# Performance work log

Measured on AMD Instinct MI355X. Metric: run time of the kernel, lower is better.

Reference implementation:

```python
import jax, jax.numpy as jnp
import numpy as np
import math

N_TERMS = 10
TWO_PI = 2.0 * math.pi


def _zernike_tables(n_terms):
    # Terms in the exact order of the torch loops: n in [0,n_terms), m in range(-n, n+1, 2).
    terms = []
    for n in range(n_terms):
        for m in range(-n, n + 1, 2):
            terms.append((n, m))
    T = len(terms)  # n_terms*(n_terms+1)/2 = 55 for n_terms=10
    C = np.zeros((T, n_terms), dtype=np.float32)  # C[t, p] = coeff of rho**p for term t
    ms = np.zeros(T, dtype=np.float32)
    for t, (n, m) in enumerate(terms):
        am = abs(m)
        for k in range((n - am) // 2 + 1):
            c = ((-1) ** k) * math.factorial(n - k) / (
                math.factorial(k)
                * math.factorial((n + am) // 2 - k)
                * math.factorial((n - am) // 2 - k)
            )
            C[t, n - 2 * k] += c
        ms[t] = m
    return C, ms


_C_NP, _MS_NP = _zernike_tables(N_TERMS)


def setup_inputs() -> dict:
    key = jax.random.key(0)
    x = jax.random.normal(key, (32, 1, 1024, 1024), dtype=jnp.float32)
    return {"x": x}


def reference(x) -> jnp.ndarray:
    # FFT features
    fft_image = jnp.fft.rfft2(x)                    # [B,1,H,Wr], Wr = W//2+1
    magnitude = jnp.abs(fft_image)
    phase = jnp.angle(fft_image)
    pu = jnp.where(phase < 0, phase + TWO_PI, phase)  # "unwrapped" phase

    # Phase gradients (torch.gradient semantics == jnp.gradient: central diff, one-sided edges)
    grad_y, grad_x = jnp.gradient(pu, axis=(2, 3))

    # Zernike coefficients over the phase map grid
    B, _, H, Wr = pu.shape
    yv = jnp.linspace(-1.0, 1.0, H)
    xv = jnp.linspace(-1.0, 1.0, Wr)
    gy, gx = jnp.meshgrid(yv, xv, indexing="ij")   # [H,Wr]
    rho = jnp.sqrt(gx ** 2 + gy ** 2)
    theta = jnp.arctan2(gy, gx)
    mask = (rho <= 1.0).astype(pu.dtype)

    C = jnp.asarray(_C_NP)                          # [T,P]
    ms = jnp.asarray(_MS_NP)                        # [T]
    powers = jnp.arange(N_TERMS, dtype=pu.dtype)    # rho**0 .. rho**(n_terms-1)
    rho_pows = rho[None] ** powers[:, None, None]   # [P,H,Wr]
    R = jnp.einsum("tp,phw->thw", C, rho_pows)     # radial polynomials, [T,H,Wr]
    mt = ms[:, None, None] * theta[None]
    ang = jnp.where(ms[:, None, None] >= 0, jnp.cos(mt), jnp.sin(-mt))
    Z = R * ang                                     # [T,H,Wr]

    pm = pu[:, 0] * mask                            # [B,H,Wr]
    coeffs = jnp.einsum("bhw,thw->bt", pm, Z) / jnp.sum(mask)  # [B,T]

    # Slope stats (torch .std is unbiased -> ddof=1)
    slope_stats = jnp.concatenate(
        [
            grad_x.mean(axis=(2, 3)),
            grad_y.mean(axis=(2, 3)),
            grad_x.std(axis=(2, 3), ddof=1),
            grad_y.std(axis=(2, 3), ddof=1),
        ],
        axis=1,
    )                                               # [B,4]

    freq_features = jnp.max(magnitude, axis=(2, 3))  # [B,1]

    return jnp.concatenate([coeffs, slope_stats, freq_features], axis=1)  # [B,60]
```

## Files before the change

kernel.cpp:

```cpp
#include <hip/hip_runtime.h>
#include <math.h>

#define BATCH 32
#define HH 1024
#define WW 1024
#define WR 513
#define NPIX (HH * WR)
#define TWO_PI_F 6.28318530717958647692f

#define LGKM_SYNC() __asm__ __volatile__("s_waitcnt lgkmcnt(0)" ::: "memory")

__device__ __forceinline__ float2 cadd(float2 a, float2 b) { return make_float2(a.x + b.x, a.y + b.y); }
__device__ __forceinline__ float2 csub(float2 a, float2 b) { return make_float2(a.x - b.x, a.y - b.y); }
__device__ __forceinline__ float2 cmul(float2 a, float2 b) {
    return make_float2(a.x * b.x - a.y * b.y, a.x * b.y + a.y * b.x);
}

__device__ __forceinline__ float fast_atan2f(float y, float x) {
    float ax = __builtin_fabsf(x), ay = __builtin_fabsf(y);
    float mx = fmaxf(ax, ay), mn = fminf(ax, ay);
    float a = mn * __builtin_amdgcn_rcpf(mx);
    float s = a * a;
    float r = fmaf(fmaf(fmaf(fmaf(0.0208351f, s, -0.085133f), s, 0.180141f),
                        s, -0.3302995f), s, 0.999866f) * a;
    if (ay > ax) r = 1.5707963268f - r;
    if (x < 0.0f) r = 3.1415926536f - r;
    return (y < 0.0f) ? -r : r;
}

__device__ __forceinline__ constexpr int ridx(int k) { return ((k & 3) << 2) | (k >> 2); }

__device__ __forceinline__ void fft16_ip(float2* d) {
    const float2 Wt1[4] = {{1.f, 0.f},
                           {0.92387953f, -0.38268343f},
                           {0.70710678f, -0.70710678f},
                           {0.38268343f, -0.92387953f}};
    const float2 Wt2[4] = {{1.f, 0.f},
                           {0.70710678f, -0.70710678f},
                           {0.f, -1.f},
                           {-0.70710678f, -0.70710678f}};
    const float2 Wt3[4] = {{1.f, 0.f},
                           {0.38268343f, -0.92387953f},
                           {-0.70710678f, -0.70710678f},
                           {-0.92387953f, 0.38268343f}};
#pragma unroll
    for (int t = 0; t < 4; ++t) {
        float2 x0 = d[t], x1 = d[t + 4], x2 = d[t + 8], x3 = d[t + 12];
        float2 a0 = cadd(x0, x2), a1 = csub(x0, x2), a2 = cadd(x1, x3), a3 = csub(x1, x3);
        d[t]      = cadd(a0, a2);
        d[t + 4]  = cmul(make_float2(a1.x + a3.y, a1.y - a3.x), Wt1[t]);
        d[t + 8]  = cmul(csub(a0, a2), Wt2[t]);
        d[t + 12] = cmul(make_float2(a1.x - a3.y, a1.y + a3.x), Wt3[t]);
    }
#pragma unroll
    for (int r = 0; r < 4; ++r) {
        float2 x0 = d[4 * r], x1 = d[4 * r + 1], x2 = d[4 * r + 2], x3 = d[4 * r + 3];
        float2 e0 = cadd(x0, x2), e1 = csub(x0, x2), e2 = cadd(x1, x3), e3 = csub(x1, x3);
        d[4 * r]     = cadd(e0, e2);
        d[4 * r + 1] = make_float2(e1.x + e3.y, e1.y - e3.x);
        d[4 * r + 2] = csub(e0, e2);
        d[4 * r + 3] = make_float2(e1.x - e3.y, e1.y + e3.x);
    }
}

__device__ __forceinline__ void twiddle_tree(float2 T, float2* Wt) {
    Wt[1] = T;
    Wt[2] = cmul(T, T);
    Wt[3] = cmul(Wt[2], T);
    Wt[4] = cmul(Wt[2], Wt[2]);
    Wt[5] = cmul(Wt[4], Wt[1]);
    Wt[6] = cmul(Wt[4], Wt[2]);
    Wt[7] = cmul(Wt[4], Wt[3]);
    Wt[8] = cmul(Wt[4], Wt[4]);
    Wt[9]  = cmul(Wt[8], Wt[1]);
    Wt[10] = cmul(Wt[8], Wt[2]);
    Wt[11] = cmul(Wt[8], Wt[3]);
    Wt[12] = cmul(Wt[8], Wt[4]);
    Wt[13] = cmul(Wt[8], Wt[5]);
    Wt[14] = cmul(Wt[8], Wt[6]);
    Wt[15] = cmul(Wt[8], Wt[7]);
}

__device__ __forceinline__ void wave_fft1024(float2* v, float2* sb, int lane) {
    fft16_ip(v);
    float s, c;
    __sincosf(-TWO_PI_F * (float)lane * (1.0f / 1024.0f), &s, &c);
    float2 Wt[16];
    twiddle_tree(make_float2(c, s), Wt);
#pragma unroll
    for (int k2 = 1; k2 < 16; ++k2) v[ridx(k2)] = cmul(v[ridx(k2)], Wt[k2]);
    const int k2p = lane & 15, qp = lane >> 4;
#pragma unroll
    for (int k2 = 0; k2 < 16; ++k2) sb[(k2 << 6) | (lane ^ k2)] = v[ridx(k2)];
    LGKM_SYNC();
#pragma unroll
    for (int m = 0; m < 16; ++m) v[m] = sb[(k2p << 6) | ((4 * m + qp) ^ k2p)];
    LGKM_SYNC();
    fft16_ip(v);
    __sincosf(-TWO_PI_F * (float)qp * (1.0f / 64.0f), &s, &c);
    twiddle_tree(make_float2(c, s), Wt);
#pragma unroll
    for (int km = 1; km < 16; ++km) v[ridx(km)] = cmul(v[ridx(km)], Wt[km]);
    const bool hi2 = (lane & 32) != 0, hi1 = (lane & 16) != 0;
#pragma unroll
    for (int m = 0; m < 16; ++m) {
        float2 a = v[m];
        float2 o = make_float2(__shfl_xor(a.x, 32, 64), __shfl_xor(a.y, 32, 64));
        float2 s1 = hi2 ? csub(o, a) : cadd(a, o);
        if (hi2 && hi1) s1 = make_float2(s1.y, -s1.x);
        float2 o2 = make_float2(__shfl_xor(s1.x, 16, 64), __shfl_xor(s1.y, 16, 64));
        v[m] = hi1 ? csub(o2, s1) : cadd(s1, o2);
    }
}

__global__ __launch_bounds__(256, 4) void row_fft_kernel(const float* __restrict__ x,
                                                         float2* __restrict__ rf2) {
    __shared__ float2 buf[4][1024];
    const int t = threadIdx.x, w = t >> 6, lane = t & 63;
    const int b = blockIdx.x >> 7;
    const int h0 = (blockIdx.x & 127) * 8;
    const float* r0 = x + ((long long)b * HH + h0 + 2 * w) * (long long)WW;
    const float* r1 = r0 + WW;
    float2 v[16];
#pragma unroll
    for (int j = 0; j < 16; ++j) v[j] = make_float2(r0[lane + 64 * j], r1[lane + 64 * j]);
    float2* mybuf = &buf[w][0];
    wave_fft1024(v, mybuf, lane);
    const int kq = 2 * ((lane >> 4) & 1) + ((lane >> 5) & 1);
    const int kbase = (lane & 15) + 256 * kq;
#pragma unroll
    for (int m = 0; m < 16; ++m) mybuf[kbase + 16 * m] = v[ridx(m)];
    __syncthreads();
    for (int idx = t; idx < 513 * 8; idx += 256) {
        int k = idx >> 3, j = idx & 7, p = j >> 1, which = j & 1;
        float2 zk = buf[p][k];
        float2 zn = buf[p][(1024 - k) & 1023];
        float2 val = which ? make_float2(0.5f * (zk.y + zn.y), 0.5f * (zn.x - zk.x))
                           : make_float2(0.5f * (zk.x + zn.x), 0.5f * (zk.y - zn.y));
        rf2[((long long)b * WR + k) * 1024 + h0 + j] = val;
    }
}

__device__ __forceinline__ constexpr int brev5(int k) {
    return ((k & 1) << 4) | ((k & 2) << 2) | (k & 4) | ((k & 8) >> 2) | ((k & 16) >> 4);
}

__device__ __forceinline__ void fft32_dif(float2* d) {
    const float2 TW[16] = {
        {1.f, 0.f},
        {0.98078528f, -0.19509032f},
        {0.92387953f, -0.38268343f},
        {0.83146961f, -0.55557023f},
        {0.70710678f, -0.70710678f},
        {0.55557023f, -0.83146961f},
        {0.38268343f, -0.92387953f},
        {0.19509032f, -0.98078528f},
        {0.f, -1.f},
        {-0.19509032f, -0.98078528f},
        {-0.38268343f, -0.92387953f},
        {-0.55557023f, -0.83146961f},
        {-0.70710678f, -0.70710678f},
        {-0.83146961f, -0.55557023f},
        {-0.92387953f, -0.38268343f},
        {-0.98078528f, -0.19509032f}};
#pragma unroll
    for (int s = 0; s < 5; ++s) {
        const int h = 16 >> s;
#pragma unroll
        for (int b = 0; b < 32; b += 2 * h) {
#pragma unroll
            for (int j = 0; j < h; ++j) {
                float2 a = d[b + j], c = d[b + j + h];
                d[b + j]     = cadd(a, c);
                d[b + j + h] = cmul(csub(a, c), TW[j << s]);
            }
        }
    }
}

__global__ __launch_bounds__(64, 4) void col_fft_kernel(float2* __restrict__ rf2,
                                                        float* __restrict__ magmax) {
    __shared__ float2 sb[2 * 1056];
    const int lane = threadIdx.x;
    const int n1 = lane & 31, row = lane >> 5;
    const long long fbase = (long long)blockIdx.x * 2;
    const long long fid = fbase + row;
    const float2* src = rf2 + fbase * 1024;

    float2 d[32];
#pragma unroll
    for (int j = 0; j < 32; ++j) d[j] = src[row * 1024 + n1 + 32 * j];

    fft32_dif(d);

    float s0, c0;
    __sincosf(-TWO_PI_F * (float)n1 * (1.0f / 1024.0f), &s0, &c0);
    const float2 Tn = make_float2(c0, s0);
    float2 ww = Tn;
#pragma unroll
    for (int k1 = 1; k1 < 32; ++k1) {
        d[brev5(k1)] = cmul(d[brev5(k1)], ww);
        if (k1 < 31) ww = cmul(ww, Tn);
    }

    float2* myLDS = sb + row * 1056;
#pragma unroll
    for (int k1 = 0; k1 < 32; ++k1) myLDS[33 * k1 + n1] = d[brev5(k1)];
    LGKM_SYNC();
#pragma unroll
    for (int j = 0; j < 32; ++j) d[j] = myLDS[33 * n1 + j];

    fft32_dif(d);

    float* pu = (float*)(rf2 + fid * 1024);
    float mmax = 0.0f;
#pragma unroll
    for (int k2 = 0; k2 < 32; ++k2) {
        float2 z = d[brev5(k2)];
        mmax = fmaxf(mmax, __builtin_amdgcn_sqrtf(z.x * z.x + z.y * z.y));
        float ph = fast_atan2f(z.y, z.x);
        pu[32 * k2 + n1] = (ph < 0.0f) ? ph + TWO_PI_F : ph;
    }
#pragma unroll
    for (int off = 16; off; off >>= 1) mmax = fmaxf(mmax, __shfl_xor(mmax, off, 64));
    if (n1 == 0) atomicMax((int*)(magmax + (int)(fid / WR)), __float_as_int(mmax));
}

#define WRED(var, idx)                                                     \
    {                                                                      \
        float r_ = var;                                                    \
        _Pragma("unroll")                                                  \
        for (int off_ = 32; off_; off_ >>= 1) r_ += __shfl_down(r_, off_); \
        if (lane == 0) red[wv * 64 + (idx)] = r_;                          \
    }

#define ZPIX(VV, YVV)                                                          \
    {                                                                          \
        const float yv_ = (YVV);                                               \
        const float r2_ = xv2 + yv_ * yv_;                                     \
        if (r2_ <= 1.0f) {                                                     \
            cnt += 1.0f;                                                       \
            const float rho = sqrtf(r2_);                                      \
            const float inv = rsqrtf(r2_);                                     \
            const float c1 = xv * inv;                                         \
            const float s1 = yv_ * inv;                                        \
            const float c2 = 2.f * c1 * c1 - 1.f;                              \
            const float c3 = 2.f * c1 * c2 - c1;                               \
            const float c4 = 2.f * c1 * c3 - c2;                               \
            const float c5 = 2.f * c1 * c4 - c3;                               \
            const float c6 = 2.f * c1 * c5 - c4;                               \
            const float c7 = 2.f * c1 * c6 - c5;                               \
            const float c8 = 2.f * c1 * c7 - c6;                               \
            const float c9 = 2.f * c1 * c8 - c7;                               \
            const float s2 = 2.f * c1 * s1;                                    \
            const float s3 = 2.f * c1 * s2 - s1;                               \
            const float s4 = 2.f * c1 * s3 - s2;                               \
            const float s5 = 2.f * c1 * s4 - s3;                               \
            const float s6 = 2.f * c1 * s5 - s4;                               \
            const float s7 = 2.f * c1 * s6 - s5;                               \
            const float s8 = 2.f * c1 * s7 - s6;                               \
            const float s9 = 2.f * c1 * s8 - s7;                               \
            const float w0 = (VV), w1 = w0 * rho, w2 = w1 * rho, w3 = w2 * rho,\
                        w4 = w3 * rho, w5 = w4 * rho, w6 = w5 * rho,           \
                        w7 = w6 * rho, w8 = w7 * rho, w9 = w8 * rho;           \
            a00 += w0;                                                         \
            a11 += w1 * c1;                                                    \
            a20 += w2;      a22 += w2 * c2;                                    \
            a31 += w3 * c1; a33 += w3 * c3;                                    \
            a40 += w4;      a42 += w4 * c2; a44 += w4 * c4;                    \
            a51 += w5 * c1; a53 += w5 * c3; a55 += w5 * c5;                    \
            a60 += w6;      a62 += w6 * c2; a64 += w6 * c4; a66 += w6 * c6;    \
            a71 += w7 * c1; a73 += w7 * c3; a75 += w7 * c5; a77 += w7 * c7;    \
            a80 += w8;      a82 += w8 * c2; a84 += w8 * c4; a86 += w8 * c6;    \
            a88 += w8 * c8;                                                    \
            a91 += w9 * c1; a93 += w9 * c3; a95 += w9 * c5; a97 += w9 * c7;    \
            a99 += w9 * c9;                                                    \
            b11 += w1 * s1;                                                    \
            b22 += w2 * s2;                                                    \
            b31 += w3 * s1; b33 += w3 * s3;                                    \
            b42 += w4 * s2; b44 += w4 * s4;                                    \
            b51 += w5 * s1; b53 += w5 * s3; b55 += w5 * s5;                    \
            b62 += w6 * s2; b64 += w6 * s4; b66 += w6 * s6;                    \
            b71 += w7 * s1; b73 += w7 * s3; b75 += w7 * s5; b77 += w7 * s7;    \
            b82 += w8 * s2; b84 += w8 * s4; b86 += w8 * s6; b88 += w8 * s8;    \
            b91 += w9 * s1; b93 += w9 * s3; b95 += w9 * s5; b97 += w9 * s7;    \
            b99 += w9 * s9;                                                    \
        }                                                                      \
    }

__global__ __launch_bounds__(256, 2) void stats_kernel(float* __restrict__ pu) {
    __shared__ float red[4 * 64];
    const int b = blockIdx.y;
    const int k0 = blockIdx.x * 9;
    const float* base = pu + (long long)b * WR * 2048;
    float a00 = 0.f, a11 = 0.f, a20 = 0.f, a22 = 0.f, a31 = 0.f, a33 = 0.f,
          a40 = 0.f, a42 = 0.f, a44 = 0.f, a51 = 0.f, a53 = 0.f, a55 = 0.f,
          a60 = 0.f, a62 = 0.f, a64 = 0.f, a66 = 0.f, a71 = 0.f, a73 = 0.f,
          a75 = 0.f, a77 = 0.f, a80 = 0.f, a82 = 0.f, a84 = 0.f, a86 = 0.f,
          a88 = 0.f, a91 = 0.f, a93 = 0.f, a95 = 0.f, a97 = 0.f, a99 = 0.f;
    float b11 = 0.f, b22 = 0.f, b31 = 0.f, b33 = 0.f, b42 = 0.f, b44 = 0.f,
          b51 = 0.f, b53 = 0.f, b55 = 0.f, b62 = 0.f, b64 = 0.f, b66 = 0.f,
          b71 = 0.f, b73 = 0.f, b75 = 0.f, b77 = 0.f, b82 = 0.f, b84 = 0.f,
          b86 = 0.f, b88 = 0.f, b91 = 0.f, b93 = 0.f, b95 = 0.f, b97 = 0.f,
          b99 = 0.f;
    float sgx = 0.f, sgx2 = 0.f, sgy = 0.f, sgy2 = 0.f, cnt = 0.f;

    const int h4 = threadIdx.x * 4;
    const float yv0 = -1.0f + (2.0f / 1023.0f) * (float)h4;
    const float ystep = 2.0f / 1023.0f;

    for (int kk = 0; kk < 9; ++kk) {
        const int k = k0 + kk;
        const float* rowc = base + (long long)k * 2048;
        const float xv = -1.0f + (1.0f / 256.0f) * (float)k;
        const float xv2 = xv * xv;

        const float4 vc = *reinterpret_cast<const float4*>(rowc + h4);
        float4 gx4;
        if (k == 0) {
            const float4 vp = *reinterpret_cast<const float4*>(rowc + 2048 + h4);
            gx4 = make_float4(vp.x - vc.x, vp.y - vc.y, vp.z - vc.z, vp.w - vc.w);
        } else if (k == WR - 1) {
            const float4 vm = *reinterpret_cast<const float4*>(rowc - 2048 + h4);
            gx4 = make_float4(vc.x - vm.x, vc.y - vm.y, vc.z - vm.z, vc.w - vm.w);
        } else {
            const float4 vm = *reinterpret_cast<const float4*>(rowc - 2048 + h4);
            const float4 vp = *reinterpret_cast<const float4*>(rowc + 2048 + h4);
            gx4 = make_float4(0.5f * (vp.x - vm.x), 0.5f * (vp.y - vm.y),
                              0.5f * (vp.z - vm.z), 0.5f * (vp.w - vm.w));
        }
        const float left  = rowc[(h4 > 0) ? h4 - 1 : 0];
        const float right = rowc[(h4 < 1020) ? h4 + 4 : 1023];
        const float gy0 = (h4 == 0)    ? vc.y - vc.x : 0.5f * (vc.y - left);
        const float gy1 = 0.5f * (vc.z - vc.x);
        const float gy2 = 0.5f * (vc.w - vc.y);
        const float gy3 = (h4 == 1020) ? vc.w - vc.z : 0.5f * (right - vc.z);

        sgx  += gx4.x + gx4.y + gx4.z + gx4.w;
        sgx2 += gx4.x * gx4.x + gx4.y * gx4.y + gx4.z * gx4.z + gx4.w * gx4.w;
        sgy  += gy0 + gy1 + gy2 + gy3;
        sgy2 += gy0 * gy0 + gy1 * gy1 + gy2 * gy2 + gy3 * gy3;

        ZPIX(vc.x, yv0);
        ZPIX(vc.y, yv0 + ystep);
        ZPIX(vc.z, yv0 + 2.0f * ystep);
        ZPIX(vc.w, yv0 + 3.0f * ystep);
    }

    const int wv = threadIdx.x >> 6, lane = threadIdx.x & 63;
    WRED(a00, 0);  WRED(a11, 1);  WRED(a20, 2);  WRED(a22, 3);  WRED(a31, 4);
    WRED(a33, 5);  WRED(a40, 6);  WRED(a42, 7);  WRED(a44, 8);  WRED(a51, 9);
    WRED(a53, 10); WRED(a55, 11); WRED(a60, 12); WRED(a62, 13); WRED(a64, 14);
    WRED(a66, 15); WRED(a71, 16); WRED(a73, 17); WRED(a75, 18); WRED(a77, 19);
    WRED(a80, 20); WRED(a82, 21); WRED(a84, 22); WRED(a86, 23); WRED(a88, 24);
    WRED(a91, 25); WRED(a93, 26); WRED(a95, 27); WRED(a97, 28); WRED(a99, 29);
    WRED(b11, 30); WRED(b22, 31); WRED(b31, 32); WRED(b33, 33); WRED(b42, 34);
    WRED(b44, 35); WRED(b51, 36); WRED(b53, 37); WRED(b55, 38); WRED(b62, 39);
    WRED(b64, 40); WRED(b66, 41); WRED(b71, 42); WRED(b73, 43); WRED(b75, 44);
    WRED(b77, 45); WRED(b82, 46); WRED(b84, 47); WRED(b86, 48); WRED(b88, 49);
    WRED(b91, 50); WRED(b93, 51); WRED(b95, 52); WRED(b97, 53); WRED(b99, 54);
    WRED(sgx, 55); WRED(sgx2, 56); WRED(sgy, 57); WRED(sgy2, 58); WRED(cnt, 59);
    __syncthreads();
    const int t = threadIdx.x;
    if (t < 60) {
        float s = red[t] + red[64 + t] + red[128 + t] + red[192 + t];
        pu[((long long)(b * 57 + blockIdx.x)) * 2048 + 1024 + t] = s;
    }
}

__device__ int moment_index(int p, int a, int is_cos) {
    int ai = 0;
    for (int pp = 0; pp < 10; ++pp)
        for (int aa = (pp & 1); aa <= pp; aa += 2) {
            if (is_cos && pp == p && aa == a) return ai;
            ++ai;
        }
    for (int pp = 1; pp < 10; ++pp)
        for (int aa = ((pp & 1) ? 1 : 2); aa <= pp; aa += 2) {
            if (!is_cos && pp == p && aa == a) return ai;
            ++ai;
        }
    return 0;
}

__device__ float factf(int n) {
    float f = 1.0f;
    for (int i = 2; i <= n; ++i) f *= (float)i;
    return f;
}

__global__ void finalize_kernel(const float* __restrict__ pu,
                                const float* __restrict__ magmax,
                                float* __restrict__ out) {
    __shared__ float abf[64];
    const int b = blockIdx.x;
    const int j = threadIdx.x;
    if (j < 60) {
        float s = 0.0f;
        for (int i = 0; i < 57; ++i)
            s += pu[((long long)(b * 57 + i)) * 2048 + 1024 + j];
        abf[j] = s;
    }
    __syncthreads();
    if (j >= 60) return;
    const float NF = (float)NPIX;
    float val;
    if (j < 55) {
        int tt = j, n = 0;
        while (tt >= n + 1) { tt -= (n + 1); ++n; }
        int m = -n + 2 * tt;
        int am = m < 0 ? -m : m;
        float s = 0.0f;
        for (int k = 0; k <= (n - am) / 2; ++k) {
            float c = factf(n - k) /
                      (factf(k) * factf((n + am) / 2 - k) * factf((n - am) / 2 - k));
            if (k & 1) c = -c;
            int p = n - 2 * k;
            s += c * abf[moment_index(p, am, m >= 0 ? 1 : 0)];
        }
        val = s / abf[59];
    } else if (j == 55) {
        val = abf[55] / NF;
    } else if (j == 56) {
        val = abf[57] / NF;
    } else if (j == 57) {
        float sum = abf[55], sq = abf[56];
        val = sqrtf(fmaxf(0.0f, (sq - sum * sum / NF) / (NF - 1.0f)));
    } else if (j == 58) {
        float sum = abf[57], sq = abf[58];
        val = sqrtf(fmaxf(0.0f, (sq - sum * sum / NF) / (NF - 1.0f)));
    } else {
        val = magmax[b];
    }
    out[b * 60 + j] = val;
}

extern "C" void kernel_launch(void* const* d_in, const int* in_sizes, int n_in,
                              void* d_out, int out_size, void* d_ws, size_t ws_size,
                              hipStream_t stream) {
    (void)in_sizes; (void)n_in; (void)out_size; (void)ws_size;
    const float* x = (const float*)d_in[0];
    float* out = (float*)d_out;

    float* magmax = (float*)d_ws;
    float2* rf2 = (float2*)((char*)d_ws + 16384);

    hipMemsetAsync(d_ws, 0, 16384, stream);
    row_fft_kernel<<<BATCH * 128, 256, 0, stream>>>(x, rf2);
    col_fft_kernel<<<8208, 64, 0, stream>>>(rf2, magmax);
    dim3 gridC(57, BATCH);
    stats_kernel<<<gridC, 256, 0, stream>>>((float*)rf2);
    finalize_kernel<<<BATCH, 64, 0, stream>>>((const float*)rf2, magmax, out);
}
```

Measured before the change: 515.8 us.

## Fuse column FFT with Zernike/slope statistics using LDS-resident phase tiles and halo columns

Merges the column-FFT kernel and the stats kernel into one. Each 256-thread block computes 8 adjacent frequency columns: 6 owned columns plus one halo column on each side. The unwrapped phase stays in shared memory, so the x-gradient, y-gradient and Zernike moments are computed without writing phase to global memory and reading it back. The LDS transpose switches from padding to an XOR swizzle. The cost is about a third more FFT work for the recomputed halo columns and 64KB of LDS per block, and the per-block partial sums are now stored into an already-consumed row of the workspace.

```diff
diff --git a/kernel.cpp b/kernel.cpp
--- a/kernel.cpp
+++ b/kernel.cpp
@@ -177,62 +177,6 @@
         }
     }
 }
-
-__global__ __launch_bounds__(64, 4) void col_fft_kernel(float2* __restrict__ rf2,
-                                                        float* __restrict__ magmax) {
-    __shared__ float2 sb[2 * 1056];
-    const int lane = threadIdx.x;
-    const int n1 = lane & 31, row = lane >> 5;
-    const long long fbase = (long long)blockIdx.x * 2;
-    const long long fid = fbase + row;
-    const float2* src = rf2 + fbase * 1024;
-
-    float2 d[32];
-#pragma unroll
-    for (int j = 0; j < 32; ++j) d[j] = src[row * 1024 + n1 + 32 * j];
-
-    fft32_dif(d);
-
-    float s0, c0;
-    __sincosf(-TWO_PI_F * (float)n1 * (1.0f / 1024.0f), &s0, &c0);
-    const float2 Tn = make_float2(c0, s0);
-    float2 ww = Tn;
-#pragma unroll
-    for (int k1 = 1; k1 < 32; ++k1) {
-        d[brev5(k1)] = cmul(d[brev5(k1)], ww);
-        if (k1 < 31) ww = cmul(ww, Tn);
-    }
-
-    float2* myLDS = sb + row * 1056;
-#pragma unroll
-    for (int k1 = 0; k1 < 32; ++k1) myLDS[33 * k1 + n1] = d[brev5(k1)];
-    LGKM_SYNC();
-#pragma unroll
-    for (int j = 0; j < 32; ++j) d[j] = myLDS[33 * n1 + j];
-
-    fft32_dif(d);
-
-    float* pu = (float*)(rf2 + fid * 1024);
-    float mmax = 0.0f;
-#pragma unroll
-    for (int k2 = 0; k2 < 32; ++k2) {
-        float2 z = d[brev5(k2)];
-        mmax = fmaxf(mmax, __builtin_amdgcn_sqrtf(z.x * z.x + z.y * z.y));
-        float ph = fast_atan2f(z.y, z.x);
-        pu[32 * k2 + n1] = (ph < 0.0f) ? ph + TWO_PI_F : ph;
-    }
-#pragma unroll
-    for (int off = 16; off; off >>= 1) mmax = fmaxf(mmax, __shfl_xor(mmax, off, 64));
-    if (n1 == 0) atomicMax((int*)(magmax + (int)(fid / WR)), __float_as_int(mmax));
-}
-
-#define WRED(var, idx)                                                     \
-    {                                                                      \
-        float r_ = var;                                                    \
-        _Pragma("unroll")                                                  \
-        for (int off_ = 32; off_; off_ >>= 1) r_ += __shfl_down(r_, off_); \
-        if (lane == 0) red[wv * 64 + (idx)] = r_;                          \
-    }
 
 #define ZPIX(VV, YVV)                                                          \
     {                                                                          \
@@ -288,11 +232,62 @@
         }                                                                      \
     }
 
-__global__ __launch_bounds__(256, 2) void stats_kernel(float* __restrict__ pu) {
-    __shared__ float red[4 * 64];
-    const int b = blockIdx.y;
-    const int k0 = blockIdx.x * 9;
-    const float* base = pu + (long long)b * WR * 2048;
+#define WRED(var, idx)                                                     \
+    {                                                                      \
+        float r_ = var;                                                    \
+        _Pragma("unroll")                                                  \
+        for (int off_ = 32; off_; off_ >>= 1) r_ += __shfl_down(r_, off_); \
+        if (lane == 0) red[w * 64 + (idx)] = r_;                           \
+    }
+
+__global__ __launch_bounds__(256, 2) void fused_col_stats_kernel(float2* __restrict__ rf2,
+                                                                 float* __restrict__ magmax) {
+    __shared__ float2 sb[8][1024];
+    float* red = (float*)&sb[0][512];
+    const int tid = threadIdx.x, w = tid >> 6, lane = tid & 63;
+    const int n1 = lane & 31, s = lane >> 5;
+    const int slot = 2 * w + s;
+    const int bx = blockIdx.x, b = blockIdx.y;
+    const int k0 = bx * 6;
+    int kf = k0 - 1 + slot;
+    kf = kf < 0 ? 0 : (kf > WR - 1 ? WR - 1 : kf);
+    const float2* src = rf2 + ((long long)b * WR + kf) * 1024;
+
+    float2 d[32];
+#pragma unroll
+    for (int j = 0; j < 32; ++j) d[j] = src[n1 + 32 * j];
+    fft32_dif(d);
+    float s0, c0;
+    __sincosf(-TWO_PI_F * (float)n1 * (1.0f / 1024.0f), &s0, &c0);
+    const float2 Tn = make_float2(c0, s0);
+    float2 ww = Tn;
+#pragma unroll
+    for (int k1 = 1; k1 < 32; ++k1) {
+        d[brev5(k1)] = cmul(d[brev5(k1)], ww);
+        if (k1 < 31) ww = cmul(ww, Tn);
+    }
+    float2* myLDS = &sb[slot][0];
+#pragma unroll
+    for (int k1 = 0; k1 < 32; ++k1) myLDS[(k1 << 5) | (n1 ^ k1)] = d[brev5(k1)];
+    LGKM_SYNC();
+#pragma unroll
+    for (int j = 0; j < 32; ++j) d[j] = myLDS[(n1 << 5) | (j ^ n1)];
+    fft32_dif(d);
+
+    float* pul_own = (float*)&sb[slot][0];
+    float mmax = 0.0f;
+#pragma unroll
+    for (int k2 = 0; k2 < 32; ++k2) {
+        float2 z = d[brev5(k2)];
+        mmax = fmaxf(mmax, __builtin_amdgcn_sqrtf(z.x * z.x + z.y * z.y));
+        float ph = fast_atan2f(z.y, z.x);
+        pul_own[32 * k2 + n1] = (ph < 0.0f) ? ph + TWO_PI_F : ph;
+    }
+#pragma unroll
+    for (int off = 16; off; off >>= 1) mmax = fmaxf(mmax, __shfl_xor(mmax, off, 64));
+    if (n1 == 0) atomicMax((int*)(magmax + b), __float_as_int(mmax));
+    __syncthreads();
+
     float a00 = 0.f, a11 = 0.f, a20 = 0.f, a22 = 0.f, a31 = 0.f, a33 = 0.f,
           a40 = 0.f, a42 = 0.f, a44 = 0.f, a51 = 0.f, a53 = 0.f, a55 = 0.f,
           a60 = 0.f, a62 = 0.f, a64 = 0.f, a66 = 0.f, a71 = 0.f, a73 = 0.f,
@@ -305,49 +300,29 @@
           b99 = 0.f;
     float sgx = 0.f, sgx2 = 0.f, sgy = 0.f, sgy2 = 0.f, cnt = 0.f;
 
-    const int h4 = threadIdx.x * 4;
-    const float yv0 = -1.0f + (2.0f / 1023.0f) * (float)h4;
-    const float ystep = 2.0f / 1023.0f;
-
-    for (int kk = 0; kk < 9; ++kk) {
-        const int k = k0 + kk;
-        const float* rowc = base + (long long)k * 2048;
+    for (int sl = 1; sl <= 6; ++sl) {
+        const int k = k0 + sl - 1;
+        if (k > WR - 1) break;
         const float xv = -1.0f + (1.0f / 256.0f) * (float)k;
         const float xv2 = xv * xv;
-
-        const float4 vc = *reinterpret_cast<const float4*>(rowc + h4);
-        float4 gx4;
-        if (k == 0) {
-            const float4 vp = *reinterpret_cast<const float4*>(rowc + 2048 + h4);
-            gx4 = make_float4(vp.x - vc.x, vp.y - vc.y, vp.z - vc.z, vp.w - vc.w);
-        } else if (k == WR - 1) {
-            const float4 vm = *reinterpret_cast<const float4*>(rowc - 2048 + h4);
-            gx4 = make_float4(vc.x - vm.x, vc.y - vm.y, vc.z - vm.z, vc.w - vm.w);
-        } else {
-            const float4 vm = *reinterpret_cast<const float4*>(rowc - 2048 + h4);
-            const float4 vp = *reinterpret_cast<const float4*>(rowc + 2048 + h4);
-            gx4 = make_float4(0.5f * (vp.x - vm.x), 0.5f * (vp.y - vm.y),
-                              0.5f * (vp.z - vm.z), 0.5f * (vp.w - vm.w));
+        const float* pc = (const float*)&sb[sl][0];
+        const float* pm = (const float*)&sb[sl - 1][0];
+        const float* pp = (const float*)&sb[sl + 1][0];
+        for (int h = tid; h < 1024; h += 256) {
+            const float v = pc[h];
+            float gx, gy;
+            if (k == 0)            gx = pp[h] - v;
+            else if (k == WR - 1)  gx = v - pm[h];
+            else                   gx = 0.5f * (pp[h] - pm[h]);
+            if (h == 0)            gy = pc[1] - v;
+            else if (h == 1023)    gy = v - pc[1022];
+            else                   gy = 0.5f * (pc[h + 1] - pc[h - 1]);
+            sgx += gx; sgx2 += gx * gx; sgy += gy; sgy2 += gy * gy;
+            const float yv = -1.0f + (2.0f / 1023.0f) * (float)h;
+            ZPIX(v, yv);
         }
-        const float left  = rowc[(h4 > 0) ? h4 - 1 : 0];
-        const float right = rowc[(h4 < 1020) ? h4 + 4 : 1023];
-        const float gy0 = (h4 == 0)    ? vc.y - vc.x : 0.5f * (vc.y - left);
-        const float gy1 = 0.5f * (vc.z - vc.x);
-        const float gy2 = 0.5f * (vc.w - vc.y);
-        const float gy3 = (h4 == 1020) ? vc.w - vc.z : 0.5f * (right - vc.z);
-
-        sgx  += gx4.x + gx4.y + gx4.z + gx4.w;
-        sgx2 += gx4.x * gx4.x + gx4.y * gx4.y + gx4.z * gx4.z + gx4.w * gx4.w;
-        sgy  += gy0 + gy1 + gy2 + gy3;
-        sgy2 += gy0 * gy0 + gy1 * gy1 + gy2 * gy2 + gy3 * gy3;
-
-        ZPIX(vc.x, yv0);
-        ZPIX(vc.y, yv0 + ystep);
-        ZPIX(vc.z, yv0 + 2.0f * ystep);
-        ZPIX(vc.w, yv0 + 3.0f * ystep);
-    }
-
-    const int wv = threadIdx.x >> 6, lane = threadIdx.x & 63;
+    }
+
     WRED(a00, 0);  WRED(a11, 1);  WRED(a20, 2);  WRED(a22, 3);  WRED(a31, 4);
     WRED(a33, 5);  WRED(a40, 6);  WRED(a42, 7);  WRED(a44, 8);  WRED(a51, 9);
     WRED(a53, 10); WRED(a55, 11); WRED(a60, 12); WRED(a62, 13); WRED(a64, 14);
@@ -361,10 +336,10 @@
     WRED(b91, 50); WRED(b93, 51); WRED(b95, 52); WRED(b97, 53); WRED(b99, 54);
     WRED(sgx, 55); WRED(sgx2, 56); WRED(sgy, 57); WRED(sgy2, 58); WRED(cnt, 59);
     __syncthreads();
-    const int t = threadIdx.x;
-    if (t < 60) {
-        float s = red[t] + red[64 + t] + red[128 + t] + red[192 + t];
-        pu[((long long)(b * 57 + blockIdx.x)) * 2048 + 1024 + t] = s;
+    if (tid < 60) {
+        float sum = red[tid] + red[64 + tid] + red[128 + tid] + red[192 + tid];
+        float* pdst = (float*)(rf2 + ((long long)b * WR + k0 + 2) * 1024);
+        pdst[tid] = sum;
     }
 }
 
@@ -389,7 +364,7 @@
     return f;
 }
 
-__global__ void finalize_kernel(const float* __restrict__ pu,
+__global__ void finalize_kernel(const float* __restrict__ rf2f,
                                 const float* __restrict__ magmax,
                                 float* __restrict__ out) {
     __shared__ float abf[64];
@@ -397,8 +372,8 @@
     const int j = threadIdx.x;
     if (j < 60) {
         float s = 0.0f;
-        for (int i = 0; i < 57; ++i)
-            s += pu[((long long)(b * 57 + i)) * 2048 + 1024 + j];
+        for (int i = 0; i < 86; ++i)
+            s += rf2f[((long long)b * WR + 6 * i + 2) * 2048 + j];
         abf[j] = s;
     }
     __syncthreads();
@@ -447,8 +422,7 @@
 
     hipMemsetAsync(d_ws, 0, 16384, stream);
     row_fft_kernel<<<BATCH * 128, 256, 0, stream>>>(x, rf2);
-    col_fft_kernel<<<8208, 64, 0, stream>>>(rf2, magmax);
-    dim3 gridC(57, BATCH);
-    stats_kernel<<<gridC, 256, 0, stream>>>((float*)rf2);
+    dim3 gridF(86, BATCH);
+    fused_col_stats_kernel<<<gridF, 256, 0, stream>>>(rf2, magmax);
     finalize_kernel<<<BATCH, 64, 0, stream>>>((const float*)rf2, magmax, out);
 }
```

Result: faster. 442.6 us (-14.2%).
